# Optimization experiments

Measured on AMD Instinct MI355X. Metric: run time of the kernel, lower is better.

The kernel has to match this reference:

```python
import jax, jax.numpy as jnp
import numpy as np

NUM_HEADS = 12
WS = 8
ROPE_BASE = 100.0  # croco/dust3r RoPE2D default frequency base


def _rope1d(t, p, inv_freq):
    # t: [Bw, h, N, d], p: [Bw, N], inv_freq: [d/2]
    freqs = p[..., None] * inv_freq                      # [Bw, N, d/2]
    emb = jnp.concatenate([freqs, freqs], axis=-1)       # [Bw, N, d]
    cos = jnp.cos(emb)[:, None, :, :]
    sin = jnp.sin(emb)[:, None, :, :]
    t1, t2 = jnp.split(t, 2, axis=-1)
    rot = jnp.concatenate([-t2, t1], axis=-1)            # rotate_half
    return t * cos + rot * sin


def _rope2d(tokens, pos):
    # tokens: [Bw, h, N, D], pos: [Bw, N, 2] (y, x). First D/2 dims use y, last D/2 use x.
    D = tokens.shape[-1]
    d = D // 2
    inv_freq = 1.0 / (ROPE_BASE ** (jnp.arange(0, d, 2, dtype=jnp.float32) / d))
    ty, tx = jnp.split(tokens, 2, axis=-1)
    return jnp.concatenate([_rope1d(ty, pos[..., 0], inv_freq),
                            _rope1d(tx, pos[..., 1], inv_freq)], axis=-1)


def setup_inputs() -> dict:
    B, H, W, C = 16, 64, 64, 768
    key = jax.random.key(0)
    ks = jax.random.split(key, 7)
    x_img = jax.random.normal(ks[0], (B, H * W, C), dtype=jnp.float32)
    yy, xx = jnp.meshgrid(jnp.arange(H), jnp.arange(W), indexing='ij')
    pos = jnp.stack([yy, xx], axis=-1).reshape(1, H * W, 2).astype(jnp.float32)
    pos2d_img = jnp.broadcast_to(pos, (B, H * W, 2))
    unseen = jax.random.normal(ks[1], (B, C), dtype=jnp.float32)
    sc = C ** -0.5
    qkv_w = jax.random.normal(ks[2], (3 * C, C), dtype=jnp.float32) * sc
    qkv_b = jax.random.normal(ks[3], (3 * C,), dtype=jnp.float32) * 0.02
    proj_w = jax.random.normal(ks[4], (C, C), dtype=jnp.float32) * sc
    proj_b = jax.random.normal(ks[5], (C,), dtype=jnp.float32) * 0.02
    return {'x_img': x_img, 'pos2d_img': pos2d_img, 'unseen': unseen,
            'qkv_w': qkv_w, 'qkv_b': qkv_b, 'proj_w': proj_w, 'proj_b': proj_b,
            'H': H, 'W': W}


def reference(x_img, pos2d_img, unseen, qkv_w, qkv_b, proj_w, proj_b, H, W):
    B, HW, C = x_img.shape
    hd = C // NUM_HEADS
    scale = hd ** -0.5
    nWh, nWw = H // WS, W // WS
    Bwin, Nwin = B * nWh * nWw, WS * WS

    # window partition
    xw = x_img.reshape(B, nWh, WS, nWw, WS, C).transpose(0, 1, 3, 2, 4, 5).reshape(Bwin, Nwin, C)
    pw = pos2d_img.reshape(B, nWh, WS, nWw, WS, 2).transpose(0, 1, 3, 2, 4, 5).reshape(Bwin, Nwin, 2)

    # append unseen token (shared across windows of an image)
    u = jnp.broadcast_to(unseen[:, None, None, :], (B, nWh * nWw, 1, C)).reshape(Bwin, 1, C)
    xw = jnp.concatenate([xw, u], axis=1)                # [Bwin, Nwin+1, C]

    qkv = xw @ qkv_w.T + qkv_b                           # [Bwin, N, 3C]
    qkv = qkv.reshape(Bwin, Nwin + 1, 3, NUM_HEADS, hd)
    q = qkv[:, :, 0].transpose(0, 2, 1, 3)               # [Bwin, h, N, hd]
    k = qkv[:, :, 1].transpose(0, 2, 1, 3)
    v = qkv[:, :, 2].transpose(0, 2, 1, 3)

    # RoPE2D on image tokens only; unseen token gets no RoPE
    q = jnp.concatenate([_rope2d(q[:, :, :Nwin], pw), q[:, :, Nwin:]], axis=2)
    k = jnp.concatenate([_rope2d(k[:, :, :Nwin], pw), k[:, :, Nwin:]], axis=2)

    attn = jax.nn.softmax(jnp.einsum('bhqd,bhkd->bhqk', q, k) * scale, axis=-1)
    out = jnp.einsum('bhqk,bhkd->bhqd', attn, v)
    out = out.transpose(0, 2, 1, 3).reshape(Bwin, Nwin + 1, C)
    out = out @ proj_w.T + proj_b

    # window merge
    out_img = out[:, :Nwin].reshape(B, nWh, nWw, WS, WS, C).transpose(0, 1, 3, 2, 4, 5).reshape(B, HW, C)
    out_unseen = out[:, Nwin].reshape(B, nWh * nWw, C).mean(axis=1)  # [B, C]
    return out_img, out_unseen
```

## Files before the change

kernel.cpp:

```cpp
#include <hip/hip_runtime.h>
#include <cstdint>
#include <cstddef>

typedef __attribute__((ext_vector_type(8)))  __bf16 bf16x8;
typedef __attribute__((ext_vector_type(4)))  float  f32x4;
typedef __attribute__((ext_vector_type(2)))  unsigned int u32x2;

#define DI __device__ __forceinline__

constexpr int Cdim = 768;
constexpr int C3   = 2304;
constexpr int NT   = 65;
constexpr int ROWS = 1024 * NT;
constexpr int ROWS_PAD = ROWS + 32;
constexpr int TP   = 96;
constexpr int PS   = 128;
constexpr long long OUT_IMG = 16LL * 4096 * 768;

DI float bf2f(unsigned short u) { unsigned int x = (unsigned int)u << 16; float f; __builtin_memcpy(&f, &x, 4); return f; }
DI unsigned short f2bf(float f) { unsigned int x; __builtin_memcpy(&x, &f, 4); x = x + 0x7fffu + ((x >> 16) & 1u); return (unsigned short)(x >> 16); }

DI void gload_lds16(const unsigned short* g, unsigned short* l) {
  __builtin_amdgcn_global_load_lds((__attribute__((address_space(1))) void*)g,
                                   (__attribute__((address_space(3))) void*)l, 16, 0, 0);
}

__global__ void k_prep(const float* __restrict__ qkv_w, const float* __restrict__ proj_w,
                       unsigned short* __restrict__ wqb, unsigned short* __restrict__ wpb,
                       float* __restrict__ rope) {
  const int NW1 = 2304 * 768;
  const int NW2 = 768 * 768;
  int total = NW1 + NW2 + 1024;
  for (int i = blockIdx.x * blockDim.x + threadIdx.x; i < total; i += gridDim.x * blockDim.x) {
    if (i < NW1) wqb[i] = f2bf(qkv_w[i]);
    else if (i < NW1 + NW2) wpb[i - NW1] = f2bf(proj_w[i - NW1]);
    else {
      int e = i - NW1 - NW2;
      int p = e >> 4, j = e & 15;
      float inv = powf(100.f, -(float)j * (1.f / 16.f));
      float a = (float)p * inv;
      rope[2 * e]     = cosf(a);
      rope[2 * e + 1] = sinf(a);
    }
  }
}

__global__ void k_xw(const float* __restrict__ x, const float* __restrict__ unseen,
                     unsigned short* __restrict__ xw) {
  int row = blockIdx.x;
  int w = row / NT, t = row - w * NT;
  const float* src;
  if (t == 64) {
    src = unseen + (size_t)(w >> 6) * Cdim;
  } else {
    int wy = (w >> 3) & 7, wx = w & 7;
    int hw = ((wy << 3) + (t >> 3)) * 64 + (wx << 3) + (t & 7);
    src = x + ((size_t)(w >> 6) * 4096 + hw) * Cdim;
  }
  float4 v = ((const float4*)src)[threadIdx.x];
  unsigned int u0 = (unsigned)f2bf(v.x) | ((unsigned)f2bf(v.y) << 16);
  unsigned int u1 = (unsigned)f2bf(v.z) | ((unsigned)f2bf(v.w) << 16);
  ((u32x2*)(xw + (size_t)row * Cdim))[threadIdx.x] = (u32x2){u0, u1};
}

template<int MODE, int NTILES>
__global__ __launch_bounds__(256, 2) void k_gemm(
    const unsigned short* __restrict__ A, const unsigned short* __restrict__ Bw,
    const float* __restrict__ bias, const float* __restrict__ rope,
    unsigned short* __restrict__ Cb, float* __restrict__ outp) {
  constexpr int K = 768;
  constexpr int NK = K / 64;
  __shared__ alignas(16) unsigned short As[256 * 64];
  __shared__ alignas(16) unsigned short Bs[128 * 64];

  constexpr int nwg = 260 * NTILES;
  constexpr int q8 = nwg / 8, r8 = nwg % 8;
  int id = blockIdx.x;
  int xcd = id & 7, lid = id >> 3;
  int wg = (xcd < r8 ? xcd * (q8 + 1) : r8 * (q8 + 1) + (xcd - r8) * q8) + lid;
  int mtile = wg / NTILES, ntile = wg - mtile * NTILES;
  int m0 = mtile * 256, n0 = ntile * 128;

  int tid = threadIdx.x;
  int lane = tid & 63, wid = tid >> 6;
  int lq = lane & 15, lg = lane >> 4;
  int wm = (wid >> 1) * 128;
  int wn = (wid & 1) * 64;

  f32x4 acc[8][4];
  #pragma unroll
  for (int i = 0; i < 8; ++i)
    #pragma unroll
    for (int j = 0; j < 4; ++j) acc[i][j] = (f32x4){0.f, 0.f, 0.f, 0.f};

  #pragma unroll 1
  for (int kt = 0; kt < NK; ++kt) {
    int k0 = kt * 64;
    #pragma unroll
    for (int j = 0; j < 8; ++j) {
      int slot = j * 256 + tid;
      int row = slot >> 3, c = slot & 7;
      gload_lds16(A + (size_t)(m0 + row) * K + k0 + (c ^ (row & 7)) * 8,
                  As + (size_t)(j * 256 + (tid & ~63)) * 8);
    }
    #pragma unroll
    for (int j = 0; j < 4; ++j) {
      int slot = j * 256 + tid;
      int row = slot >> 3, c = slot & 7;
      gload_lds16(Bw + (size_t)(n0 + row) * K + k0 + (c ^ (row & 7)) * 8,
                  Bs + (size_t)(j * 256 + (tid & ~63)) * 8);
    }
    __syncthreads();

    bf16x8 bfr[8];
    #pragma unroll
    for (int nf = 0; nf < 4; ++nf)
      #pragma unroll
      for (int ks = 0; ks < 2; ++ks) {
        int row = wn + nf * 16 + lq;
        bfr[nf * 2 + ks] = *(const bf16x8*)(Bs + row * 64 + (((ks * 4 + lg) ^ (row & 7)) * 8));
      }
    #pragma unroll
    for (int half = 0; half < 2; ++half) {
      bf16x8 af[8];
      #pragma unroll
      for (int mf = 0; mf < 4; ++mf)
        #pragma unroll
        for (int ks = 0; ks < 2; ++ks) {
          int row = wm + half * 64 + mf * 16 + lq;
          af[mf * 2 + ks] = *(const bf16x8*)(As + row * 64 + (((ks * 4 + lg) ^ (row & 7)) * 8));
        }
      #pragma unroll
      for (int mf = 0; mf < 4; ++mf)
        #pragma unroll
        for (int nf = 0; nf < 4; ++nf)
          #pragma unroll
          for (int ks = 0; ks < 2; ++ks)
            acc[half * 4 + mf][nf] =
              __builtin_amdgcn_mfma_f32_16x16x32_bf16(af[mf * 2 + ks], bfr[nf * 2 + ks],
                                                      acc[half * 4 + mf][nf], 0, 0, 0);
    }
    __syncthreads();
  }

  #pragma unroll
  for (int mf = 0; mf < 8; ++mf) {
    #pragma unroll
    for (int r = 0; r < 4; ++r) {
      int row = m0 + wm + mf * 16 + (lg << 2) + r;
      int w = row / NT, t = row - w * NT;
      int wy = (w >> 3) & 7, wx = w & 7;
      int py = (wy << 3) + (t >> 3), px = (wx << 3) + (t & 7);
      #pragma unroll
      for (int a = 0; a < 2; ++a) {
        int col0 = n0 + wn + a * 32 + lq;
        int col1 = col0 + 16;
        float v0 = acc[mf][2 * a][r] + bias[col0];
        float v1 = acc[mf][2 * a + 1][r] + bias[col1];
        if (MODE == 0) {
          if (col0 < 1536 && t != 64) {
            int p = a ? px : py;
            const float* rp = rope + ((p << 4) + lq) * 2;
            float cc = rp[0], ss = rp[1];
            float o0 = v0 * cc - v1 * ss;
            float o1 = v1 * cc + v0 * ss;
            v0 = o0; v1 = o1;
          }
          unsigned short* cr = Cb + (size_t)row * C3;
          cr[col0] = f2bf(v0);
          cr[col1] = f2bf(v1);
        } else {
          if (t == 64) {
            float* ub = outp + OUT_IMG + (size_t)(w >> 6) * Cdim;
            atomicAdd(ub + col0, v0 * (1.f / 64.f));
            atomicAdd(ub + col1, v1 * (1.f / 64.f));
          } else {
            float* orow = outp + ((size_t)(w >> 6) * 4096 + py * 64 + px) * Cdim;
            orow[col0] = v0;
            orow[col1] = v1;
          }
        }
      }
    }
  }
}

__global__ void k_vt(const unsigned short* __restrict__ qkv, unsigned short* __restrict__ Vt) {
  int bh = blockIdx.x;
  int w = bh / 12, h = bh - w * 12;
  __shared__ float sv[65][65];
  const unsigned short* base = qkv + (size_t)w * NT * C3 + 1536 + h * 64;
  for (int i = threadIdx.x; i < 65 * 64; i += 256) {
    int t = i >> 6, d = i & 63;
    sv[t][d] = bf2f(base[(size_t)t * C3 + d]);
  }
  __syncthreads();
  unsigned short* out = Vt + (size_t)bh * 64 * TP;
  for (int i = threadIdx.x; i < 64 * TP; i += 256) {
    int d = i / TP, t = i - d * TP;
    out[i] = f2bf(t < 65 ? sv[t][d] : 0.f);
  }
}

__global__ __launch_bounds__(64) void k_attn(const unsigned short* __restrict__ qkv,
                                             const unsigned short* __restrict__ Vt,
                                             unsigned short* __restrict__ att) {
  __shared__ alignas(16) unsigned short P[80 * PS];
  int h = blockIdx.x, w = blockIdx.y;
  int lane = threadIdx.x;
  int lq = lane & 15, lg = lane >> 4;

  const unsigned short* qb = qkv + (size_t)w * NT * C3 + h * 64;
  const unsigned short* kb = qb + 768;

  bf16x8 kf[5][2];
  #pragma unroll
  for (int kt = 0; kt < 5; ++kt)
    #pragma unroll
    for (int ks = 0; ks < 2; ++ks)
      kf[kt][ks] = *(const bf16x8*)(kb + (size_t)(kt * 16 + lq) * C3 + ks * 32 + lg * 8);

  const unsigned short* vb = Vt + (size_t)(w * 12 + h) * 64 * TP;
  bf16x8 vf[3][4];
  #pragma unroll
  for (int ks = 0; ks < 3; ++ks)
    #pragma unroll
    for (int dt = 0; dt < 4; ++dt)
      vf[ks][dt] = *(const bf16x8*)(vb + (size_t)(dt * 16 + lq) * TP + ks * 32 + lg * 8);

  for (int i = lane; i < 80 * 8; i += 64) {
    int row = i >> 3, j = i & 7;
    int byteo = row * (PS * 2) + 160 + j * 4;
    byteo ^= (row & 7) << 4;
    *(unsigned int*)((char*)P + byteo) = 0u;
  }

  #pragma unroll 1
  for (int qt = 0; qt < 5; ++qt) {
    bf16x8 qf[2];
    #pragma unroll
    for (int ks = 0; ks < 2; ++ks)
      qf[ks] = *(const bf16x8*)(qb + (size_t)(qt * 16 + lq) * C3 + ks * 32 + lg * 8);

    f32x4 sa[5];
    #pragma unroll
    for (int kt = 0; kt < 5; ++kt) {
      sa[kt] = (f32x4){0.f, 0.f, 0.f, 0.f};
      #pragma unroll
      for (int ks = 0; ks < 2; ++ks)
        sa[kt] = __builtin_amdgcn_mfma_f32_16x16x32_bf16(kf[kt][ks], qf[ks], sa[kt], 0, 0, 0);
    }
    float pv[5][4];
    float m = -1e30f;
    #pragma unroll
    for (int kt = 0; kt < 5; ++kt)
      #pragma unroll
      for (int r = 0; r < 4; ++r) {
        int tok = kt * 16 + lg * 4 + r;
        float s = sa[kt][r] * 0.125f;
        bool ok = tok < 65;
        pv[kt][r] = ok ? s : -1e30f;
        m = (ok && s > m) ? s : m;
      }
    m = fmaxf(m, __shfl_xor(m, 16));
    m = fmaxf(m, __shfl_xor(m, 32));
    float sum = 0.f;
    #pragma unroll
    for (int kt = 0; kt < 5; ++kt)
      #pragma unroll
      for (int r = 0; r < 4; ++r) {
        float e = (pv[kt][r] > -1e29f) ? exp2f((pv[kt][r] - m) * 1.44269504f) : 0.f;
        pv[kt][r] = e;
        sum += e;
      }
    sum += __shfl_xor(sum, 16);
    sum += __shfl_xor(sum, 32);
    float rinv = 1.f / sum;

    int q = qt * 16 + lq;
    #pragma unroll
    for (int kt = 0; kt < 5; ++kt) {
      unsigned int u0 = (unsigned)f2bf(pv[kt][0] * rinv) | ((unsigned)f2bf(pv[kt][1] * rinv) << 16);
      unsigned int u1 = (unsigned)f2bf(pv[kt][2] * rinv) | ((unsigned)f2bf(pv[kt][3] * rinv) << 16);
      int byteo = q * (PS * 2) + kt * 32 + lg * 8;
      byteo ^= (q & 7) << 4;
      *(u32x2*)((char*)P + byteo) = (u32x2){u0, u1};
    }
    asm volatile("s_waitcnt lgkmcnt(0)" ::: "memory");

    bf16x8 bp[3];
    #pragma unroll
    for (int ks = 0; ks < 3; ++ks) {
      int byteo = q * (PS * 2) + ks * 64 + lg * 16;
      byteo ^= (q & 7) << 4;
      bp[ks] = *(const bf16x8*)((char*)P + byteo);
    }
    #pragma unroll
    for (int dt = 0; dt < 4; ++dt) {
      f32x4 o = (f32x4){0.f, 0.f, 0.f, 0.f};
      #pragma unroll
      for (int ks = 0; ks < 3; ++ks)
        o = __builtin_amdgcn_mfma_f32_16x16x32_bf16(vf[ks][dt], bp[ks], o, 0, 0, 0);
      if (q < 65) {
        unsigned int u0 = (unsigned)f2bf(o[0]) | ((unsigned)f2bf(o[1]) << 16);
        unsigned int u1 = (unsigned)f2bf(o[2]) | ((unsigned)f2bf(o[3]) << 16);
        *(u32x2*)(att + (size_t)(w * NT + q) * Cdim + h * 64 + dt * 16 + lg * 4) = (u32x2){u0, u1};
      }
    }
  }
}

extern "C" void kernel_launch(void* const* d_in, const int* in_sizes, int n_in,
                              void* d_out, int out_size, void* d_ws, size_t ws_size,
                              hipStream_t stream) {
  const float* x_img  = (const float*)d_in[0];
  const float* unseen = (const float*)d_in[2];
  const float* qkv_w  = (const float*)d_in[3];
  const float* qkv_b  = (const float*)d_in[4];
  const float* proj_w = (const float*)d_in[5];
  const float* proj_b = (const float*)d_in[6];

  char* ws = (char*)d_ws;
  size_t off = 0;
  auto alloc = [&](size_t bytes) { void* p = ws + off; off = (off + bytes + 255) & ~(size_t)255; return p; };
  unsigned short* xw  = (unsigned short*)alloc((size_t)ROWS * Cdim * 2);
  unsigned short* qkv = (unsigned short*)alloc((size_t)ROWS_PAD * C3 * 2);
  unsigned short* Vt  = (unsigned short*)alloc((size_t)12288 * 64 * TP * 2);
  unsigned short* wqb = (unsigned short*)alloc((size_t)C3 * Cdim * 2);
  unsigned short* wpb = (unsigned short*)alloc((size_t)Cdim * Cdim * 2);
  float* rope = (float*)alloc(64 * 16 * 2 * sizeof(float));

  hipMemsetAsync((float*)d_out + OUT_IMG, 0, 16 * Cdim * sizeof(float), stream);

  k_prep<<<512, 256, 0, stream>>>(qkv_w, proj_w, wqb, wpb, rope);
  k_xw<<<ROWS, 192, 0, stream>>>(x_img, unseen, xw);
  k_gemm<0, 18><<<260 * 18, 256, 0, stream>>>(xw, wqb, qkv_b, rope, qkv, nullptr);
  k_vt<<<12288, 256, 0, stream>>>(qkv, Vt);
  k_attn<<<dim3(12, 1024), 64, 0, stream>>>(qkv, Vt, xw);
  k_gemm<1, 6><<<260 * 6, 256, 0, stream>>>(xw, wpb, proj_b, nullptr, nullptr, (float*)d_out);
}
```

Baseline: 725.3 us.

## Double-buffer GEMM K-loop and stage epilogue through LDS for coalesced stores

The GEMM K loop now uses 32-wide K steps with two LDS buffers, issuing the next tile's global-to-LDS loads before computing the current one, so loads overlap MFMA work. The epilogue writes results into a swizzled LDS tile and then stores 16-byte vectors to global memory instead of scattered 2- and 4-byte stores. The V-transpose kernel also packs eight bf16 values per 16-byte store. This trades a larger LDS footprint and extra syncs in the epilogue for better memory-level overlap and coalescing.

```diff
diff --git a/kernel.cpp b/kernel.cpp
--- a/kernel.cpp
+++ b/kernel.cpp
@@ -5,6 +5,7 @@
 typedef __attribute__((ext_vector_type(8)))  __bf16 bf16x8;
 typedef __attribute__((ext_vector_type(4)))  float  f32x4;
 typedef __attribute__((ext_vector_type(2)))  unsigned int u32x2;
+typedef __attribute__((ext_vector_type(4)))  unsigned int u32x4;
 
 #define DI __device__ __forceinline__
 
@@ -69,9 +70,8 @@
     const float* __restrict__ bias, const float* __restrict__ rope,
     unsigned short* __restrict__ Cb, float* __restrict__ outp) {
   constexpr int K = 768;
-  constexpr int NK = K / 64;
-  __shared__ alignas(16) unsigned short As[256 * 64];
-  __shared__ alignas(16) unsigned short Bs[128 * 64];
+  constexpr int NK = 24;
+  __shared__ alignas(16) unsigned short lds[32768];
 
   constexpr int nwg = 260 * NTILES;
   constexpr int q8 = nwg / 8, r8 = nwg % 8;
@@ -87,77 +87,81 @@
   int wm = (wid >> 1) * 128;
   int wn = (wid & 1) * 64;
 
+  auto stage = [&](int kt, int b) {
+    unsigned short* dA = lds + b * 12288;
+    unsigned short* dB = dA + 8192;
+    int k0 = kt * 32;
+    #pragma unroll
+    for (int j = 0; j < 4; ++j) {
+      int ch = j * 256 + tid;
+      int row = ch >> 2, kc = ch & 3;
+      int skc = kc ^ ((row >> 1) & 3);
+      gload_lds16(A + (size_t)(m0 + row) * K + k0 + skc * 8,
+                  dA + (size_t)(j * 256 + (tid & ~63)) * 8);
+    }
+    #pragma unroll
+    for (int j = 0; j < 2; ++j) {
+      int ch = j * 256 + tid;
+      int row = ch >> 2, kc = ch & 3;
+      int skc = kc ^ ((row >> 1) & 3);
+      gload_lds16(Bw + (size_t)(n0 + row) * K + k0 + skc * 8,
+                  dB + (size_t)(j * 256 + (tid & ~63)) * 8);
+    }
+  };
+
   f32x4 acc[8][4];
   #pragma unroll
   for (int i = 0; i < 8; ++i)
     #pragma unroll
     for (int j = 0; j < 4; ++j) acc[i][j] = (f32x4){0.f, 0.f, 0.f, 0.f};
 
-  #pragma unroll 1
-  for (int kt = 0; kt < NK; ++kt) {
-    int k0 = kt * 64;
-    #pragma unroll
-    for (int j = 0; j < 8; ++j) {
-      int slot = j * 256 + tid;
-      int row = slot >> 3, c = slot & 7;
-      gload_lds16(A + (size_t)(m0 + row) * K + k0 + (c ^ (row & 7)) * 8,
-                  As + (size_t)(j * 256 + (tid & ~63)) * 8);
-    }
-    #pragma unroll
-    for (int j = 0; j < 4; ++j) {
-      int slot = j * 256 + tid;
-      int row = slot >> 3, c = slot & 7;
-      gload_lds16(Bw + (size_t)(n0 + row) * K + k0 + (c ^ (row & 7)) * 8,
-                  Bs + (size_t)(j * 256 + (tid & ~63)) * 8);
-    }
+  auto compute = [&](int b) {
+    const unsigned short* sA = lds + b * 12288;
+    const unsigned short* sB = sA + 8192;
+    bf16x8 af[8], bfr[4];
+    #pragma unroll
+    for (int mf = 0; mf < 8; ++mf) {
+      int row = wm + mf * 16 + lq;
+      af[mf] = *(const bf16x8*)(sA + row * 32 + ((lg ^ ((row >> 1) & 3)) * 8));
+    }
+    #pragma unroll
+    for (int nf = 0; nf < 4; ++nf) {
+      int row = wn + nf * 16 + lq;
+      bfr[nf] = *(const bf16x8*)(sB + row * 32 + ((lg ^ ((row >> 1) & 3)) * 8));
+    }
+    #pragma unroll
+    for (int mf = 0; mf < 8; ++mf)
+      #pragma unroll
+      for (int nf = 0; nf < 4; ++nf)
+        acc[mf][nf] = __builtin_amdgcn_mfma_f32_16x16x32_bf16(af[mf], bfr[nf], acc[mf][nf], 0, 0, 0);
+  };
+
+  stage(0, 0);
+  __syncthreads();
+  #pragma unroll 2
+  for (int t = 0; t < NK; ++t) {
+    if (t + 1 < NK) stage(t + 1, (t + 1) & 1);
+    compute(t & 1);
     __syncthreads();
-
-    bf16x8 bfr[8];
-    #pragma unroll
-    for (int nf = 0; nf < 4; ++nf)
-      #pragma unroll
-      for (int ks = 0; ks < 2; ++ks) {
-        int row = wn + nf * 16 + lq;
-        bfr[nf * 2 + ks] = *(const bf16x8*)(Bs + row * 64 + (((ks * 4 + lg) ^ (row & 7)) * 8));
-      }
-    #pragma unroll
-    for (int half = 0; half < 2; ++half) {
-      bf16x8 af[8];
-      #pragma unroll
-      for (int mf = 0; mf < 4; ++mf)
+  }
+
+  if (MODE == 0) {
+    unsigned short* ct = lds;
+    #pragma unroll
+    for (int mf = 0; mf < 8; ++mf) {
+      #pragma unroll
+      for (int r = 0; r < 4; ++r) {
+        int lrow = wm + mf * 16 + (lg << 2) + r;
+        int grow = m0 + lrow;
+        int w = grow / NT, t = grow - w * NT;
+        int wy = (w >> 3) & 7, wx = w & 7;
+        int py = (wy << 3) + (t >> 3), px = (wx << 3) + (t & 7);
         #pragma unroll
-        for (int ks = 0; ks < 2; ++ks) {
-          int row = wm + half * 64 + mf * 16 + lq;
-          af[mf * 2 + ks] = *(const bf16x8*)(As + row * 64 + (((ks * 4 + lg) ^ (row & 7)) * 8));
-        }
-      #pragma unroll
-      for (int mf = 0; mf < 4; ++mf)
-        #pragma unroll
-        for (int nf = 0; nf < 4; ++nf)
-          #pragma unroll
-          for (int ks = 0; ks < 2; ++ks)
-            acc[half * 4 + mf][nf] =
-              __builtin_amdgcn_mfma_f32_16x16x32_bf16(af[mf * 2 + ks], bfr[nf * 2 + ks],
-                                                      acc[half * 4 + mf][nf], 0, 0, 0);
-    }
-    __syncthreads();
-  }
-
-  #pragma unroll
-  for (int mf = 0; mf < 8; ++mf) {
-    #pragma unroll
-    for (int r = 0; r < 4; ++r) {
-      int row = m0 + wm + mf * 16 + (lg << 2) + r;
-      int w = row / NT, t = row - w * NT;
-      int wy = (w >> 3) & 7, wx = w & 7;
-      int py = (wy << 3) + (t >> 3), px = (wx << 3) + (t & 7);
-      #pragma unroll
-      for (int a = 0; a < 2; ++a) {
-        int col0 = n0 + wn + a * 32 + lq;
-        int col1 = col0 + 16;
-        float v0 = acc[mf][2 * a][r] + bias[col0];
-        float v1 = acc[mf][2 * a + 1][r] + bias[col1];
-        if (MODE == 0) {
+        for (int a = 0; a < 2; ++a) {
+          int cn0 = wn + a * 32 + lq;
+          int col0 = n0 + cn0, col1 = col0 + 16;
+          float v0 = acc[mf][2 * a][r] + bias[col0];
+          float v1 = acc[mf][2 * a + 1][r] + bias[col1];
           if (col0 < 1536 && t != 64) {
             int p = a ? px : py;
             const float* rp = rope + ((p << 4) + lq) * 2;
@@ -166,21 +170,68 @@
             float o1 = v1 * cc + v0 * ss;
             v0 = o0; v1 = o1;
           }
-          unsigned short* cr = Cb + (size_t)row * C3;
-          cr[col0] = f2bf(v0);
-          cr[col1] = f2bf(v1);
-        } else {
-          if (t == 64) {
-            float* ub = outp + OUT_IMG + (size_t)(w >> 6) * Cdim;
-            atomicAdd(ub + col0, v0 * (1.f / 64.f));
-            atomicAdd(ub + col1, v1 * (1.f / 64.f));
-          } else {
-            float* orow = outp + ((size_t)(w >> 6) * 4096 + py * 64 + px) * Cdim;
-            orow[col0] = v0;
-            orow[col1] = v1;
+          int b0 = (lrow * 256 + cn0 * 2) ^ ((lrow & 7) << 4);
+          int b1 = (lrow * 256 + (cn0 + 16) * 2) ^ ((lrow & 7) << 4);
+          *(unsigned short*)((char*)ct + b0) = f2bf(v0);
+          *(unsigned short*)((char*)ct + b1) = f2bf(v1);
+        }
+      }
+    }
+    __syncthreads();
+    #pragma unroll
+    for (int j = 0; j < 16; ++j) {
+      int idx = j * 256 + tid;
+      int row = idx >> 4, c = idx & 15;
+      u32x4 v = *(const u32x4*)((char*)ct + row * 256 + ((c ^ (row & 7)) << 4));
+      *(u32x4*)(Cb + (size_t)(m0 + row) * C3 + n0 + c * 8) = v;
+    }
+  } else {
+    float* cf = (float*)lds;
+    #pragma unroll
+    for (int half = 0; half < 2; ++half) {
+      if ((wm >> 7) == half) {
+        #pragma unroll
+        for (int mf = 0; mf < 8; ++mf) {
+          #pragma unroll
+          for (int r = 0; r < 4; ++r) {
+            int lrow = mf * 16 + (lg << 2) + r;
+            int grow = m0 + half * 128 + lrow;
+            int w = grow / NT, t = grow - w * NT;
+            #pragma unroll
+            for (int a = 0; a < 2; ++a) {
+              int cn0 = wn + a * 32 + lq;
+              int col0 = n0 + cn0, col1 = col0 + 16;
+              float v0 = acc[mf][2 * a][r] + bias[col0];
+              float v1 = acc[mf][2 * a + 1][r] + bias[col1];
+              if (t == 64) {
+                float* ub = outp + OUT_IMG + (size_t)(w >> 6) * Cdim;
+                atomicAdd(ub + col0, v0 * (1.f / 64.f));
+                atomicAdd(ub + col1, v1 * (1.f / 64.f));
+              } else {
+                int b0 = (lrow * 512 + cn0 * 4) ^ ((lrow & 7) << 4);
+                int b1 = (lrow * 512 + (cn0 + 16) * 4) ^ ((lrow & 7) << 4);
+                *(float*)((char*)cf + b0) = v0;
+                *(float*)((char*)cf + b1) = v1;
+              }
+            }
           }
         }
       }
+      __syncthreads();
+      #pragma unroll
+      for (int j = 0; j < 16; ++j) {
+        int idx = j * 256 + tid;
+        int row = idx >> 5, c = idx & 31;
+        int grow = m0 + half * 128 + row;
+        int w = grow / NT, t = grow - w * NT;
+        if (t != 64) {
+          int wy = (w >> 3) & 7, wx = w & 7;
+          int py = (wy << 3) + (t >> 3), px = (wx << 3) + (t & 7);
+          u32x4 v = *(const u32x4*)((char*)cf + row * 512 + ((c ^ (row & 7)) << 4));
+          *(u32x4*)(outp + ((size_t)(w >> 6) * 4096 + py * 64 + px) * Cdim + n0 + c * 4) = v;
+        }
+      }
+      __syncthreads();
     }
   }
 }
@@ -196,9 +247,18 @@
   }
   __syncthreads();
   unsigned short* out = Vt + (size_t)bh * 64 * TP;
-  for (int i = threadIdx.x; i < 64 * TP; i += 256) {
-    int d = i / TP, t = i - d * TP;
-    out[i] = f2bf(t < 65 ? sv[t][d] : 0.f);
+  for (int i = threadIdx.x; i < 64 * (TP / 8); i += 256) {
+    int d = i / (TP / 8), tc = i - d * (TP / 8);
+    int t0 = tc * 8;
+    unsigned int u[4];
+    #pragma unroll
+    for (int k = 0; k < 4; ++k) {
+      int ta = t0 + 2 * k, tb = ta + 1;
+      unsigned short sa = (ta < 65) ? f2bf(sv[ta][d]) : (unsigned short)0;
+      unsigned short sb = (tb < 65) ? f2bf(sv[tb][d]) : (unsigned short)0;
+      u[k] = (unsigned)sa | ((unsigned)sb << 16);
+    }
+    *(u32x4*)(out + d * TP + t0) = (u32x4){u[0], u[1], u[2], u[3]};
   }
 }
 
```

Result: no change. 719.4 us (-0.8%).
